# Kernel optimization log

Hardware: AMD Instinct MI355X
Metric: run time of the kernel (lower is better)

Reference implementation:

```python
import jax, jax.numpy as jnp
import numpy as np

DIM_MODEL = 1024
HEADS = 16
DIM_PER_HEAD = DIM_MODEL // HEADS


def setup_inputs() -> dict:
    key = jax.random.key(0)
    k0, k1, k2, k3, k4 = jax.random.split(key, 5)
    x = jax.random.normal(k0, (2, 2048, DIM_MODEL), dtype=jnp.float32)
    # combined_linear: dim_model -> 3*dim_model (torch Linear: y = x @ W.T + b)
    s_in = 1.0 / np.sqrt(DIM_MODEL)
    W_qkv = jax.random.uniform(k1, (3 * DIM_MODEL, DIM_MODEL), minval=-s_in, maxval=s_in, dtype=jnp.float32)
    b_qkv = jax.random.uniform(k2, (3 * DIM_MODEL,), minval=-s_in, maxval=s_in, dtype=jnp.float32)
    W_out = jax.random.uniform(k3, (DIM_MODEL, DIM_MODEL), minval=-s_in, maxval=s_in, dtype=jnp.float32)
    b_out = jax.random.uniform(k4, (DIM_MODEL,), minval=-s_in, maxval=s_in, dtype=jnp.float32)
    return {"x": x, "W_qkv": W_qkv, "b_qkv": b_qkv, "W_out": W_out, "b_out": b_out}


def reference(x, W_qkv, b_qkv, W_out, b_out):
    B, S, D = x.shape
    H, Dh = HEADS, DIM_PER_HEAD
    qkv = x @ W_qkv.T + b_qkv  # [B, S, 3D]
    q, k, v = jnp.split(qkv, 3, axis=2)
    # [B, H, S, Dh]
    q = q.reshape(B, S, H, Dh).transpose(0, 2, 1, 3)
    k = k.reshape(B, S, H, Dh).transpose(0, 2, 1, 3)
    v = v.reshape(B, S, H, Dh).transpose(0, 2, 1, 3)
    scores = jnp.einsum('bhqd,bhkd->bhqk', q, k) / jnp.sqrt(jnp.float32(Dh))
    causal = jnp.tril(jnp.ones((S, S), dtype=bool))
    scores = jnp.where(causal[None, None, :, :], scores, -jnp.inf)
    p_attn = jax.nn.softmax(scores, axis=-1)
    out = jnp.einsum('bhqk,bhkd->bhqd', p_attn, v)
    out = out.transpose(0, 2, 1, 3).reshape(B, S, D)
    return out @ W_out.T + b_out
```

## Files before the change

kernel.cpp:

```cpp
#include <hip/hip_runtime.h>
#include <cstdint>

typedef __attribute__((ext_vector_type(8))) __bf16 bf16x8;
typedef __attribute__((ext_vector_type(4))) float f32x4;
typedef __attribute__((ext_vector_type(8))) short short8;
typedef __attribute__((ext_vector_type(4))) float float4v;
typedef __attribute__((ext_vector_type(4))) unsigned uint4v;
typedef __attribute__((ext_vector_type(4))) unsigned short ushort4v;

__device__ __forceinline__ unsigned short f2bf(float f) {
    unsigned u = __builtin_bit_cast(unsigned, f);
    u += 0x7fffu + ((u >> 16) & 1u);
    return (unsigned short)(u >> 16);
}
__device__ __forceinline__ float bf2f(unsigned short s) {
    return __builtin_bit_cast(float, (unsigned)s << 16);
}
__device__ __forceinline__ f32x4 mfma_bf16(bf16x8 a, bf16x8 b, f32x4 c) {
    return __builtin_amdgcn_mfma_f32_16x16x32_bf16(a, b, c, 0, 0, 0);
}
__device__ __forceinline__ unsigned pkbf(float lo, float hi) {
    unsigned r;
    asm("v_cvt_pk_bf16_f32 %0, %1, %2" : "=v"(r) : "v"(lo), "v"(hi));
    return r;
}

#define GLD16(g, l)                                                                     \
    __builtin_amdgcn_global_load_lds((const __attribute__((address_space(1))) void*)(g), \
                                     (__attribute__((address_space(3))) void*)(l), 16, 0, 0)

__global__ void __launch_bounds__(256) cvt_f32_bf16(const float* __restrict__ src,
                                                    unsigned short* __restrict__ dst, int n8) {
    const int stride = gridDim.x * blockDim.x;
    for (int i = blockIdx.x * blockDim.x + threadIdx.x; i < n8; i += stride) {
        const float4v* s = (const float4v*)(src + (size_t)i * 8);
        float4v v0 = s[0], v1 = s[1];
        short8 o;
        o[0] = (short)f2bf(v0[0]); o[1] = (short)f2bf(v0[1]);
        o[2] = (short)f2bf(v0[2]); o[3] = (short)f2bf(v0[3]);
        o[4] = (short)f2bf(v1[0]); o[5] = (short)f2bf(v1[1]);
        o[6] = (short)f2bf(v1[2]); o[7] = (short)f2bf(v1[3]);
        *(short8*)(dst + (size_t)i * 8) = o;
    }
}

template <int MODE>
__global__ void __launch_bounds__(256) gemm_bt(const unsigned short* __restrict__ A,
                                               const unsigned short* __restrict__ B,
                                               const float* __restrict__ bias,
                                               void* __restrict__ C,
                                               unsigned short* __restrict__ vT,
                                               int M, int N, int K) {
    __shared__ __attribute__((aligned(16))) unsigned short As[2][128 * 32];
    __shared__ __attribute__((aligned(16))) unsigned short Bs[2][128 * 32];
    const int tid = threadIdx.x;
    const int w = tid >> 6, lane = tid & 63;
    const int a = lane & 15, g = lane >> 4;
    const int m0 = blockIdx.y * 128, n0 = blockIdx.x * 128;
    const int wr = (w >> 1) * 64, wc = (w & 1) * 64;

    f32x4 acc[4][4];
#pragma unroll
    for (int i = 0; i < 4; i++)
#pragma unroll
        for (int j = 0; j < 4; j++) acc[i][j] = (f32x4)(0.0f);

    const int r0 = tid >> 2;
    const int c0 = (tid & 3) * 8;
    const unsigned short* gA0 = A + (size_t)(m0 + r0) * K + c0;
    const unsigned short* gA1 = A + (size_t)(m0 + 64 + r0) * K + c0;
    const unsigned short* gB0 = B + (size_t)(n0 + r0) * K + c0;
    const unsigned short* gB1 = B + (size_t)(n0 + 64 + r0) * K + c0;

#define GSTAGE(buf_, k0_)                                               \
    {                                                                   \
        char* la_ = (char*)&As[buf_][0] + w * 1024;                     \
        char* lb_ = (char*)&Bs[buf_][0] + w * 1024;                     \
        GLD16(gA0 + (k0_), la_);                                        \
        GLD16(gA1 + (k0_), la_ + 4096);                                 \
        GLD16(gB0 + (k0_), lb_);                                        \
        GLD16(gB1 + (k0_), lb_ + 4096);                                 \
    }

    GSTAGE(0, 0);
    __syncthreads();

    int cur = 0;
    for (int k0 = 0; k0 < K; k0 += 32) {
        if (k0 + 32 < K) GSTAGE(cur ^ 1, k0 + 32);

        bf16x8 af[4], bfr[4];
#pragma unroll
        for (int i = 0; i < 4; i++) {
            af[i]  = *(const bf16x8*)&As[cur][(wr + i * 16 + a) * 32 + g * 8];
            bfr[i] = *(const bf16x8*)&Bs[cur][(wc + i * 16 + a) * 32 + g * 8];
        }
#pragma unroll
        for (int i = 0; i < 4; i++)
#pragma unroll
            for (int j = 0; j < 4; j++) acc[i][j] = mfma_bf16(af[i], bfr[j], acc[i][j]);

        __syncthreads();
        cur ^= 1;
    }
#undef GSTAGE

#pragma unroll
    for (int j = 0; j < 4; j++) {
        const int col = n0 + wc + j * 16 + a;
        const float bv = bias[col];
        if (MODE == 0) {
            float* Cf = (float*)C;
#pragma unroll
            for (int i = 0; i < 4; i++)
#pragma unroll
                for (int jr = 0; jr < 4; jr++) {
                    const int row = m0 + wr + i * 16 + g * 4 + jr;
                    Cf[(size_t)row * N + col] = acc[i][j][jr] + bv;
                }
        } else if (n0 < 2048) {
            unsigned short* Cb = (unsigned short*)C;
#pragma unroll
            for (int i = 0; i < 4; i++)
#pragma unroll
                for (int jr = 0; jr < 4; jr++) {
                    const int row = m0 + wr + i * 16 + g * 4 + jr;
                    Cb[(size_t)row * 2048 + col] = f2bf(acc[i][j][jr] + bv);
                }
        } else {
            const int vd = col - 2048;
            const int hh = vd >> 6, dd = vd & 63;
#pragma unroll
            for (int i = 0; i < 4; i++) {
                const int token0 = m0 + wr + i * 16 + g * 4;
                const int bb = token0 >> 11, kl = token0 & 2047;
                ushort4v st;
#pragma unroll
                for (int jr = 0; jr < 4; jr++) st[jr] = f2bf(acc[i][j][jr] + bv);
                *(ushort4v*)(vT + ((size_t)((bb << 4) + hh) * 64 + dd) * 2048 + kl) = st;
            }
        }
    }
}


#define STAGE(bf_, t_)                                                  \
    {                                                                   \
        const size_t ko_ = (size_t)(t_) * 128 * LDQ;                    \
        const size_t vo_ = (size_t)(t_) * 128;                          \
        char* db_ = (char*)&KV[bf_][0] + w * 1024;                      \
        GLD16(sK0 + ko_, db_);                                          \
        GLD16(sK1 + ko_, db_ + 8192);                                   \
        GLD16(sV0 + vo_, db_ + 16384);                                  \
        GLD16(sV1 + vo_, db_ + 24576);                                  \
    }

__global__ void __launch_bounds__(512, 4) attn_fwd(const unsigned short* __restrict__ qk,
                                                   const unsigned short* __restrict__ vT,
                                                   unsigned short* __restrict__ o) {
    constexpr int SL = 2048, DH = 64, LDQ = 2048;
    constexpr float GAMMA = 0.18033688011112042f;
    const int bh = blockIdx.x & 31;
    const int s = blockIdx.x >> 5;
    const int qb = (s < 8) ? 15 - s : s - 8;
    const int b = bh >> 4, h = bh & 15;
    const int tid = threadIdx.x;
    const int w = tid >> 6, lane = tid & 63;
    const int n = lane & 15, g = lane >> 4;

    __shared__ __attribute__((aligned(16))) unsigned short KV[2][16384];

    const int qs = qb * 128 + w * 16 + n;
    const int nt = qb + 1;

    bf16x8 qf[2];
    {
        const unsigned short* qp = qk + (size_t)(b * SL + qs) * LDQ + h * DH + g * 8;
        short8 la = *(const short8*)qp, lb = *(const short8*)(qp + 32);
        short8 s0, s1;
#pragma unroll
        for (int e = 0; e < 8; e++) {
            s0[e] = (short)f2bf(bf2f((unsigned short)la[e]) * GAMMA);
            s1[e] = (short)f2bf(bf2f((unsigned short)lb[e]) * GAMMA);
        }
        qf[0] = __builtin_bit_cast(bf16x8, s0);
        qf[1] = __builtin_bit_cast(bf16x8, s1);
    }

    const int rK = tid >> 3;
    const int xrK = (rK & 3) | (((rK >> 3) & 1) << 2);
    const int csK = (((tid & 7) ^ xrK) << 3);
    const unsigned short* sK0 = qk + (size_t)(b * SL + rK) * LDQ + 1024 + h * DH + csK;
    const unsigned short* sK1 = sK0 + (size_t)64 * LDQ;
    const int dV = tid >> 4;
    const int csV = (((tid & 15) ^ (dV & 7)) << 3);
    const unsigned short* sV0 = vT + (size_t)bh * DH * SL + (size_t)dV * SL + csV;
    const unsigned short* sV1 = sV0 + (size_t)32 * SL;

    const int srow = 8 * (n >> 2) + (n & 3);
    const int xrq = (n & 3) | (((n >> 2) & 1) << 2);
    const int offK0 = ((g ^ xrq) << 3);
    const int offK1 = offK0 ^ 32;
    int offV[4];
#pragma unroll
    for (int kc = 0; kc < 4; kc++) offV[kc] = (((4 * kc + g) ^ (n & 7)) << 3);

    f32x4 of[4];
#pragma unroll
    for (int i = 0; i < 4; i++) of[i] = (f32x4)(0.0f);
    float m_i = -1e30f, l_i = 0.0f;

    STAGE(0, 0);
    __syncthreads();

    for (int t = 0; t < nt; ++t) {
        const unsigned short* kvb = &KV[t & 1][0];
        if (t + 1 < nt) STAGE((t & 1) ^ 1, t + 1);

        f32x4 p[8];
#pragma unroll
        for (int f = 0; f < 8; f++) {
            const int r_ = srow + ((f >> 1) << 5) + ((f & 1) << 2);
            const bf16x8 ka_ = *(const bf16x8*)&kvb[r_ * 64 + offK0];
            const bf16x8 kc_ = *(const bf16x8*)&kvb[r_ * 64 + offK1];
            f32x4 acc_ = (f32x4)(0.0f);
            acc_ = mfma_bf16(ka_, qf[0], acc_);
            acc_ = mfma_bf16(kc_, qf[1], acc_);
            p[f] = acc_;
        }

        if (t == nt - 1) {
            const int k0 = t * 128;
#pragma unroll
            for (int f = 0; f < 8; f++) {
                const int kb_ = k0 + ((f >> 1) << 5) + ((f & 1) << 2) + 8 * g;
#pragma unroll
                for (int e = 0; e < 4; e++)
                    if (kb_ + e > qs) p[f][e] = -1e30f;
            }
        }

        float mx = -1e30f;
#pragma unroll
        for (int f = 0; f < 8; f++) {
            const float a_ = fmaxf(fmaxf(p[f][0], p[f][1]), fmaxf(p[f][2], p[f][3]));
            mx = fmaxf(mx, a_);
        }
        mx = fmaxf(mx, __shfl_xor(mx, 16));
        mx = fmaxf(mx, __shfl_xor(mx, 32));
        if (!__all(mx <= m_i + 8.0f)) {
            const float mn_ = fmaxf(m_i, mx);
            const float al_ = __builtin_amdgcn_exp2f(m_i - mn_);
            l_i *= al_;
#pragma unroll
            for (int d_ = 0; d_ < 4; d_++) of[d_] = of[d_] * al_;
            m_i = mn_;
        }
        float rs = 0.0f;
#pragma unroll
        for (int f = 0; f < 8; f++)
#pragma unroll
            for (int e = 0; e < 4; e++) {
                p[f][e] = __builtin_amdgcn_exp2f(p[f][e] - m_i);
                rs += p[f][e];
            }
        l_i += rs;

        bf16x8 pf[4];
#pragma unroll
        for (int kc = 0; kc < 4; kc++) {
            uint4v u_;
            u_[0] = pkbf(p[2 * kc][0], p[2 * kc][1]);
            u_[1] = pkbf(p[2 * kc][2], p[2 * kc][3]);
            u_[2] = pkbf(p[2 * kc + 1][0], p[2 * kc + 1][1]);
            u_[3] = pkbf(p[2 * kc + 1][2], p[2 * kc + 1][3]);
            pf[kc] = __builtin_bit_cast(bf16x8, u_);
        }

        const unsigned short* vb = kvb + 8192;
#pragma unroll
        for (int df = 0; df < 4; df++) {
            const int vrow = (df * 16 + n) * 128;
#pragma unroll
            for (int kc = 0; kc < 4; kc++) {
                const bf16x8 va_ = *(const bf16x8*)&vb[vrow + offV[kc]];
                of[df] = mfma_bf16(va_, pf[kc], of[df]);
            }
        }

        __syncthreads();
    }

    float rl = l_i;
    rl += __shfl_xor(rl, 16);
    rl += __shfl_xor(rl, 32);
    const float inv = 1.0f / rl;
    unsigned short* op = o + (size_t)(b * SL + qs) * 1024 + h * DH + 4 * g;
#pragma unroll
    for (int df = 0; df < 4; df++) {
        ushort4v st;
#pragma unroll
        for (int r = 0; r < 4; r++) st[r] = f2bf(of[df][r] * inv);
        *(ushort4v*)(op + df * 16) = st;
    }
}

extern "C" void kernel_launch(void* const* d_in, const int* in_sizes, int n_in,
                              void* d_out, int out_size, void* d_ws, size_t ws_size,
                              hipStream_t stream) {
    (void)in_sizes; (void)n_in; (void)out_size; (void)ws_size;
    const float* x    = (const float*)d_in[0];
    const float* Wqkv = (const float*)d_in[1];
    const float* bqkv = (const float*)d_in[2];
    const float* Wout = (const float*)d_in[3];
    const float* bout = (const float*)d_in[4];
    float* out = (float*)d_out;

    const int BS = 2, SL = 2048, DM = 1024;
    const int M = BS * SL;
    const int N1 = 3 * DM;
    const int K = DM;

    char* ws = (char*)d_ws;
    unsigned short* x_bf    = (unsigned short*)(ws);
    unsigned short* wqkv_bf = (unsigned short*)(ws + (8u << 20));
    unsigned short* wout_bf = (unsigned short*)(ws + (14u << 20));
    unsigned short* qkbuf   = (unsigned short*)(ws + (16u << 20));
    unsigned short* vTbuf   = (unsigned short*)(ws + (32u << 20));
    unsigned short* attn_o  = (unsigned short*)(ws + (40u << 20));

    cvt_f32_bf16<<<2048, 256, 0, stream>>>(x, x_bf, M * K / 8);
    cvt_f32_bf16<<<1536, 256, 0, stream>>>(Wqkv, wqkv_bf, N1 * K / 8);
    cvt_f32_bf16<<<512, 256, 0, stream>>>(Wout, wout_bf, DM * DM / 8);

    gemm_bt<1><<<dim3(N1 / 128, M / 128), 256, 0, stream>>>(x_bf, wqkv_bf, bqkv, qkbuf, vTbuf, M, N1, K);

    attn_fwd<<<dim3(512), 512, 0, stream>>>(qkbuf, vTbuf, attn_o);

    gemm_bt<0><<<dim3(DM / 128, M / 128), 256, 0, stream>>>(attn_o, wout_bf, bout, out, nullptr, M, DM, K);
}
```

Measured before the change: 108.2 us.

## Fuse conversion kernels, remap GEMM tiles per XCD, raise MFMA priority

Merges the three f32-to-bf16 conversion launches into one kernel that uses packed bf16 convert instructions, removing two launches. Both GEMMs move to a 1D grid with a remap that places neighbouring tiles on the same XCD chiplet (blockIdx mod 8), aiming for better L2 reuse. The attention kernel raises wave priority around its MFMA sections so matrix work is favoured over other waves. The GEMM remap hardcodes 32 M-tiles (by = nf & 31) and relies on the grid size being a multiple of 8.

```diff
diff --git a/kernel.cpp b/kernel.cpp
--- a/kernel.cpp
+++ b/kernel.cpp
@@ -29,18 +29,29 @@
     __builtin_amdgcn_global_load_lds((const __attribute__((address_space(1))) void*)(g), \
                                      (__attribute__((address_space(3))) void*)(l), 16, 0, 0)
 
-__global__ void __launch_bounds__(256) cvt_f32_bf16(const float* __restrict__ src,
-                                                    unsigned short* __restrict__ dst, int n8) {
-    const int stride = gridDim.x * blockDim.x;
-    for (int i = blockIdx.x * blockDim.x + threadIdx.x; i < n8; i += stride) {
-        const float4v* s = (const float4v*)(src + (size_t)i * 8);
-        float4v v0 = s[0], v1 = s[1];
-        short8 o;
-        o[0] = (short)f2bf(v0[0]); o[1] = (short)f2bf(v0[1]);
-        o[2] = (short)f2bf(v0[2]); o[3] = (short)f2bf(v0[3]);
-        o[4] = (short)f2bf(v1[0]); o[5] = (short)f2bf(v1[1]);
-        o[6] = (short)f2bf(v1[2]); o[7] = (short)f2bf(v1[3]);
-        *(short8*)(dst + (size_t)i * 8) = o;
+__global__ void __launch_bounds__(256) cvt_all(const float* __restrict__ x,
+                                               const float* __restrict__ wqkv,
+                                               const float* __restrict__ wout,
+                                               unsigned short* __restrict__ xb,
+                                               unsigned short* __restrict__ wqb,
+                                               unsigned short* __restrict__ wob) {
+    int i = blockIdx.x * blockDim.x + threadIdx.x;
+#pragma unroll
+    for (int k = 0; k < 2; k++, i += 524288) {
+        const float* s;
+        unsigned short* d;
+        int off;
+        if (i < 524288)      { s = x;    d = xb;  off = i; }
+        else if (i < 917504) { s = wqkv; d = wqb; off = i - 524288; }
+        else                 { s = wout; d = wob; off = i - 917504; }
+        const float4v* sp = (const float4v*)(s + (size_t)off * 8);
+        float4v v0 = sp[0], v1 = sp[1];
+        uint4v u;
+        u[0] = pkbf(v0[0], v0[1]);
+        u[1] = pkbf(v0[2], v0[3]);
+        u[2] = pkbf(v1[0], v1[1]);
+        u[3] = pkbf(v1[2], v1[3]);
+        *(uint4v*)(d + (size_t)off * 8) = u;
     }
 }
 
@@ -56,7 +67,12 @@
     const int tid = threadIdx.x;
     const int w = tid >> 6, lane = tid & 63;
     const int a = lane & 15, g = lane >> 4;
-    const int m0 = blockIdx.y * 128, n0 = blockIdx.x * 128;
+
+    const int cpx = gridDim.x >> 3;
+    const int nf = ((int)blockIdx.x & 7) * cpx + ((int)blockIdx.x >> 3);
+    const int bx = nf >> 5;
+    const int by = nf & 31;
+    const int m0 = by * 128, n0 = bx * 128;
     const int wr = (w >> 1) * 64, wc = (w & 1) * 64;
 
     f32x4 acc[4][4];
@@ -218,6 +234,7 @@
         if (t + 1 < nt) STAGE((t & 1) ^ 1, t + 1);
 
         f32x4 p[8];
+        __builtin_amdgcn_s_setprio(1);
 #pragma unroll
         for (int f = 0; f < 8; f++) {
             const int r_ = srow + ((f >> 1) << 5) + ((f & 1) << 2);
@@ -228,6 +245,7 @@
             acc_ = mfma_bf16(kc_, qf[1], acc_);
             p[f] = acc_;
         }
+        __builtin_amdgcn_s_setprio(0);
 
         if (t == nt - 1) {
             const int k0 = t * 128;
@@ -278,6 +296,7 @@
         }
 
         const unsigned short* vb = kvb + 8192;
+        __builtin_amdgcn_s_setprio(1);
 #pragma unroll
         for (int df = 0; df < 4; df++) {
             const int vrow = (df * 16 + n) * 128;
@@ -287,6 +306,7 @@
                 of[df] = mfma_bf16(va_, pf[kc], of[df]);
             }
         }
+        __builtin_amdgcn_s_setprio(0);
 
         __syncthreads();
     }
@@ -329,13 +349,11 @@
     unsigned short* vTbuf   = (unsigned short*)(ws + (32u << 20));
     unsigned short* attn_o  = (unsigned short*)(ws + (40u << 20));
 
-    cvt_f32_bf16<<<2048, 256, 0, stream>>>(x, x_bf, M * K / 8);
-    cvt_f32_bf16<<<1536, 256, 0, stream>>>(Wqkv, wqkv_bf, N1 * K / 8);
-    cvt_f32_bf16<<<512, 256, 0, stream>>>(Wout, wout_bf, DM * DM / 8);
-
-    gemm_bt<1><<<dim3(N1 / 128, M / 128), 256, 0, stream>>>(x_bf, wqkv_bf, bqkv, qkbuf, vTbuf, M, N1, K);
+    cvt_all<<<2048, 256, 0, stream>>>(x, Wqkv, Wout, x_bf, wqkv_bf, wout_bf);
+
+    gemm_bt<1><<<dim3(N1 / 128 * (M / 128)), 256, 0, stream>>>(x_bf, wqkv_bf, bqkv, qkbuf, vTbuf, M, N1, K);
 
     attn_fwd<<<dim3(512), 512, 0, stream>>>(qkbuf, vTbuf, attn_o);
 
-    gemm_bt<0><<<dim3(DM / 128, M / 128), 256, 0, stream>>>(attn_o, wout_bf, bout, out, nullptr, M, DM, K);
-}
+    gemm_bt<0><<<dim3(DM / 128 * (M / 128)), 256, 0, stream>>>(attn_o, wout_bf, bout, out, nullptr, M, DM, K);
+}
```

New measurement: 105.1 us. 2.9% less time.
